# Kernel optimization log

Hardware: AMD Instinct MI355X
Metric: run time of the kernel (lower is better)

The kernel has to match this reference:

```python
import jax, jax.numpy as jnp
import numpy as np


def _conv1d(x, w, b, groups=1):
    # x: (B, Cin, N); w: (Cout, Cin//groups, K)
    pad = (w.shape[-1] - 1) // 2
    y = jax.lax.conv_general_dilated(
        x, w, window_strides=(1,), padding=[(pad, pad)],
        feature_group_count=groups, dimension_numbers=("NCH", "OIH", "NCH"))
    return y + b[None, :, None]


def _conv2d_1x1(x, w, b, groups=1):
    # x: (B, Cin, H, W); w: (Cout, Cin//groups, 1, 1)
    y = jax.lax.conv_general_dilated(
        x, w, window_strides=(1, 1), padding=[(0, 0), (0, 0)],
        feature_group_count=groups, dimension_numbers=("NCHW", "OIHW", "NCHW"))
    return y + b[None, :, None, None]


def setup_inputs() -> dict:
    key = jax.random.key(0)
    ks = jax.random.split(key, 13)
    B, C, N = 16, 256, 2048
    W, G = 128, 32  # width = 4 * groups
    s = 0.05
    inp = {"x": jax.random.normal(ks[0], (B, C, N), jnp.float32)}
    # tconvs: Conv1d(C,W,1) -> Conv1d(W,W,3,groups=G) -> Conv1d(W,C,1)
    inp["Wt1"] = jax.random.normal(ks[1], (W, C, 1), jnp.float32) * s
    inp["bt1"] = jax.random.normal(ks[2], (W,), jnp.float32) * s
    inp["Wt2"] = jax.random.normal(ks[3], (W, W // G, 3), jnp.float32) * s
    inp["bt2"] = jax.random.normal(ks[4], (W,), jnp.float32) * s
    inp["Wt3"] = jax.random.normal(ks[5], (C, W, 1), jnp.float32) * s
    inp["bt3"] = jax.random.normal(ks[6], (C,), jnp.float32) * s
    # sconvs: Conv2d(2C,W,1) -> Conv2d(W,W,1,groups=G) -> Conv2d(W,C,1)
    inp["Ws1"] = jax.random.normal(ks[7], (W, 2 * C, 1, 1), jnp.float32) * s
    inp["bs1"] = jax.random.normal(ks[8], (W,), jnp.float32) * s
    inp["Ws2"] = jax.random.normal(ks[9], (W, W // G, 1, 1), jnp.float32) * s
    inp["bs2"] = jax.random.normal(ks[10], (W,), jnp.float32) * s
    inp["Ws3"] = jax.random.normal(ks[11], (C, W, 1, 1), jnp.float32) * s
    inp["bs3"] = jax.random.normal(ks[12], (C,), jnp.float32) * s
    return inp


def reference(x, Wt1, bt1, Wt2, bt2, Wt3, bt3, Ws1, bs1, Ws2, bs2, Ws3, bs3):
    K, G = 3, 32
    B, C, N = x.shape
    # --- temporal branch (tconvs) ---
    t = jax.nn.relu(_conv1d(x, Wt1, bt1))
    t = jax.nn.relu(_conv1d(t, Wt2, bt2, groups=G))
    tout = _conv1d(t, Wt3, bt3)  # (B, C, N)
    # --- knn: pd[b,m,n] = -||x_m - x_n||^2; top-k largest = k nearest ---
    sq = jnp.sum(x * x, axis=1)  # (B, N)
    pd = 2.0 * jnp.einsum("bcm,bcn->bmn", x, x) - sq[:, :, None] - sq[:, None, :]
    idx = jax.lax.top_k(pd, K)[1]  # (B, N, K)
    # --- gather neighbors, style=1: cat(neighbor, center) ---
    xt = jnp.transpose(x, (0, 2, 1))  # (B, N, C)
    neigh = jax.vmap(lambda xb, ib: xb[ib])(xt, idx)  # (B, N, K, C)
    center = jnp.broadcast_to(xt[:, :, None, :], neigh.shape)
    feat = jnp.transpose(jnp.concatenate([neigh, center], axis=3), (0, 3, 1, 2))  # (B, 2C, N, K)
    # --- semantic branch (sconvs) + max over neighbors ---
    s1 = jax.nn.relu(_conv2d_1x1(feat, Ws1, bs1))
    s1 = jax.nn.relu(_conv2d_1x1(s1, Ws2, bs2, groups=G))
    sout = _conv2d_1x1(s1, Ws3, bs3).max(axis=-1)  # (B, C, N)
    return jax.nn.relu(tout + x + sout)
```

## Files before the change

### kernel.cpp

```cpp
#include <hip/hip_runtime.h>

#define DI __device__ __forceinline__

typedef float f4 __attribute__((ext_vector_type(4)));
typedef float f2 __attribute__((ext_vector_type(2)));
typedef unsigned short u16x8 __attribute__((ext_vector_type(8)));
typedef unsigned short u16x4 __attribute__((ext_vector_type(4)));
typedef __bf16 bf16x8 __attribute__((ext_vector_type(8)));
typedef float f32x4 __attribute__((ext_vector_type(4)));

constexpr int C = 256;
constexpr int N = 2048;
constexpr int BN = 16 * 2048;

DI float bf2f(unsigned short h){
  union { unsigned int u; float f; } v; v.u = ((unsigned int)h) << 16; return v.f;
}
DI unsigned short f2bf(float f){
  union { float f; unsigned int u; } v; v.f = f;
  unsigned int r = v.u + 0x7fffu + ((v.u >> 16) & 1u);
  return (unsigned short)(r >> 16);
}
DI unsigned int f2u(float f){ union { float f; unsigned int u; } v; v.f = f; return v.u; }
DI float u2f(unsigned int u){ union { unsigned int u; float f; } v; v.u = u; return v.f; }

DI void ins3(float v, int n, float& v0, float& v1, float& v2, int& i0, int& i1, int& i2){
  bool b0 = (v > v0) || (v == v0 && n < i0);
  bool b1 = (v > v1) || (v == v1 && n < i1);
  bool b2 = (v > v2) || (v == v2 && n < i2);
  if (b0){ v2=v1; i2=i1; v1=v0; i1=i0; v0=v; i0=n; }
  else if (b1){ v2=v1; i2=i1; v1=v; i1=n; }
  else if (b2){ v2=v; i2=n; }
}

DI void gload16(const void* g, void* l){
  __builtin_amdgcn_global_load_lds(
      (const __attribute__((address_space(1))) unsigned int*)g,
      (__attribute__((address_space(3))) unsigned int*)l, 16, 0, 0);
}

__global__ __launch_bounds__(256) void k_cvt(const float* __restrict__ x,
    unsigned short* __restrict__ xhT, float* __restrict__ xT, float* __restrict__ sq4)
{
  __shared__ float T[64][68];
  int bid = blockIdx.x;
  int pt = bid & 31, ct = (bid >> 5) & 3, b = bid >> 7;
  int p0 = pt * 64, c0 = ct * 64;
  int tid = threadIdx.x;
  int cr = tid >> 4, cv = tid & 15;
  const float* xb = x + ((size_t)b * C + c0) * N + p0;
  #pragma unroll
  for (int i = 0; i < 4; i++){
    int c = cr + i * 16;
    f4 v = *(const f4*)(xb + (size_t)c * N + cv * 4);
    T[cv*4+0][c] = v[0]; T[cv*4+1][c] = v[1]; T[cv*4+2][c] = v[2]; T[cv*4+3][c] = v[3];
  }
  __syncthreads();
  int p = tid >> 2, cq = tid & 3;
  size_t rowg = (size_t)b * N + p0 + p;
  float* xtr = xT + rowg * 256 + c0 + cq * 16;
  unsigned short* xhr = xhT + rowg * 256 + c0 + cq * 16;
  float sacc = 0.f;
  #pragma unroll
  for (int j = 0; j < 4; j++){
    f4 v = *(const f4*)&T[p][cq*16 + j*4];
    *(f4*)(xtr + j*4) = v;
    sacc += (v[0]*v[0] + v[1]*v[1]) + (v[2]*v[2] + v[3]*v[3]);
    u16x4 h; h[0]=f2bf(v[0]); h[1]=f2bf(v[1]); h[2]=f2bf(v[2]); h[3]=f2bf(v[3]);
    *(u16x4*)(xhr + j*4) = h;
  }
  sacc += __shfl_xor(sacc, 1, 64);
  sacc += __shfl_xor(sacc, 2, 64);
  if (cq == 0) sq4[rowg * 4 + ct] = sacc;
}

__global__ __launch_bounds__(256, 2) void k_pd(const unsigned short* __restrict__ xhT,
    const float* __restrict__ sq4, int* __restrict__ idx8)
{
  __shared__ __align__(16) char sm[81920];
  int wg = blockIdx.x;
  int wid = (wg & 7) * 64 + (wg >> 3);
  int b = wid >> 5, mt = wid & 31;
  int m0 = mt * 64;
  int tid = threadIdx.x, w = tid >> 6, l = tid & 63;
  const unsigned short* xb = xhT + (size_t)b * N * 256;
  const float* sqb4 = sq4 + (size_t)b * N * 4;
  char* Ab = sm + 49152;
  char* wbuf = sm + w * 12288;

  #pragma unroll
  for (int i = 0; i < 8; i++){
    int flat = i * 256 + tid;
    int m = flat >> 5, c = flat & 31;
    gload16(xb + (size_t)(m0 + m) * 256 + ((c ^ (m & 7)) << 3), Ab + flat * 16);
  }
  #pragma unroll
  for (int t = 0; t < 2; t++){
    #pragma unroll
    for (int i = 0; i < 4; i++){
      int p = i * 4 + (l >> 4), c = l & 15;
      gload16(xb + (size_t)(w * 16 + p) * 256 + t * 128 + ((c ^ (p & 7)) << 3),
              wbuf + t * 4096 + (i * 64 + l) * 16);
    }
  }
  asm volatile("s_waitcnt vmcnt(8)" ::: "memory");
  __builtin_amdgcn_s_barrier();

  bf16x8 af[4][8];
  #pragma unroll
  for (int rt = 0; rt < 4; rt++)
    #pragma unroll
    for (int ks = 0; ks < 8; ks++){
      int m = rt * 16 + (l & 15);
      int ch = ks * 4 + (l >> 4);
      af[rt][ks] = *(const bf16x8*)(Ab + m * 512 + ((ch ^ (m & 7)) << 4));
    }

  float K[16][3];
  #pragma unroll
  for (int a = 0; a < 16; a++){ K[a][0] = 0.f; K[a][1] = 0.f; K[a][2] = 0.f; }

  f32x4 acc[4];
  for (int it = 0; it < 64; it++){
    if (it < 62){
      int nx = it + 2;
      int P0 = (nx >> 1) * 64, kh2 = nx & 1;
      char* dst = wbuf + (nx % 3) * 4096;
      #pragma unroll
      for (int i = 0; i < 4; i++){
        int p = i * 4 + (l >> 4), c = l & 15;
        gload16(xb + (size_t)(P0 + w * 16 + p) * 256 + kh2 * 128 + ((c ^ (p & 7)) << 3),
                dst + (i * 64 + l) * 16);
      }
    }
    if (it < 62)       asm volatile("s_waitcnt vmcnt(8)" ::: "memory");
    else if (it == 62) asm volatile("s_waitcnt vmcnt(4)" ::: "memory");
    else               asm volatile("s_waitcnt vmcnt(0)" ::: "memory");

    const char* bb = wbuf + (it % 3) * 4096;
    int kh = it & 1;
    if (kh == 0){
      f32x4 z = {0.f, 0.f, 0.f, 0.f};
      #pragma unroll
      for (int rt = 0; rt < 4; rt++) acc[rt] = z;
    }
    #pragma unroll
    for (int ks = 0; ks < 4; ks++){
      int p = l & 15;
      int ch = ks * 4 + (l >> 4);
      bf16x8 bv = *(const bf16x8*)(bb + p * 256 + ((ch ^ (p & 7)) << 4));
      if (kh == 0){
        #pragma unroll
        for (int rt = 0; rt < 4; rt++)
          acc[rt] = __builtin_amdgcn_mfma_f32_16x16x32_bf16(af[rt][ks], bv, acc[rt], 0, 0, 0);
      } else {
        #pragma unroll
        for (int rt = 0; rt < 4; rt++)
          acc[rt] = __builtin_amdgcn_mfma_f32_16x16x32_bf16(af[rt][4 + ks], bv, acc[rt], 0, 0, 0);
      }
    }
    if (kh == 1){
      int col = (it >> 1) * 64 + w * 16 + (l & 15);
      f4 s4 = *(const f4*)(sqb4 + (size_t)col * 4);
      float nb = 1024.f - ((s4[0] + s4[1]) + (s4[2] + s4[3]));
      unsigned int ib = (unsigned int)(2047 - col);
      #pragma unroll
      for (int rt = 0; rt < 4; rt++)
        #pragma unroll
        for (int r = 0; r < 4; r++){
          float v = fmaf(acc[rt][r], 2.f, nb);
          float key = u2f((f2u(v) & 0xFFFFF800u) | ib);
          int a = rt * 4 + r;
          K[a][2] = __builtin_amdgcn_fmed3f(K[a][1], K[a][2], key);
          K[a][1] = __builtin_amdgcn_fmed3f(K[a][0], K[a][1], key);
          K[a][0] = fmaxf(K[a][0], key);
        }
    }
  }
  __syncthreads();
  float* mK = (float*)sm;
  #pragma unroll
  for (int rt = 0; rt < 4; rt++)
    #pragma unroll
    for (int r = 0; r < 4; r++){
      int row = rt * 16 + (l >> 4) * 4 + r;
      int base = row * 193 + w * 48 + (l & 15) * 3;
      mK[base+0] = K[rt*4+r][0]; mK[base+1] = K[rt*4+r][1]; mK[base+2] = K[rt*4+r][2];
    }
  __syncthreads();
  float* aux = (float*)(sm + 49408);
  {
    int row = tid >> 2, q = tid & 3;
    float t0 = 0.f, t1 = 0.f, t2 = 0.f, t3 = 0.f;
    const float* src = mK + row * 193 + q * 48;
    for (int s = 0; s < 48; s++){
      float v = src[s];
      t3 = __builtin_amdgcn_fmed3f(t2, t3, v);
      t2 = __builtin_amdgcn_fmed3f(t1, t2, v);
      t1 = __builtin_amdgcn_fmed3f(t0, t1, v);
      t0 = fmaxf(t0, v);
    }
    float* d = aux + row * 17 + q * 4;
    d[0] = t0; d[1] = t1; d[2] = t2; d[3] = t3;
  }
  __syncthreads();
  if (tid < 64){
    float u0=0.f,u1=0.f,u2=0.f,u3=0.f,u4=0.f,u5=0.f,u6=0.f,u7=0.f;
    const float* srcp = aux + tid * 17;
    #pragma unroll
    for (int s = 0; s < 16; s++){
      float v = srcp[s];
      u7 = __builtin_amdgcn_fmed3f(u6, u7, v);
      u6 = __builtin_amdgcn_fmed3f(u5, u6, v);
      u5 = __builtin_amdgcn_fmed3f(u4, u5, v);
      u4 = __builtin_amdgcn_fmed3f(u3, u4, v);
      u3 = __builtin_amdgcn_fmed3f(u2, u3, v);
      u2 = __builtin_amdgcn_fmed3f(u1, u2, v);
      u1 = __builtin_amdgcn_fmed3f(u0, u1, v);
      u0 = fmaxf(u0, v);
    }
    int* d = idx8 + ((size_t)(b * N + m0 + tid)) * 8;
    d[0]=2047-(int)(f2u(u0)&2047u); d[1]=2047-(int)(f2u(u1)&2047u);
    d[2]=2047-(int)(f2u(u2)&2047u); d[3]=2047-(int)(f2u(u3)&2047u);
    d[4]=2047-(int)(f2u(u4)&2047u); d[5]=2047-(int)(f2u(u5)&2047u);
    d[6]=2047-(int)(f2u(u6)&2047u); d[7]=2047-(int)(f2u(u7)&2047u);
  }
}

__global__ __launch_bounds__(256) void k_rerank(const float* __restrict__ xT,
    const float* __restrict__ sq4, const int* __restrict__ idx8, int* __restrict__ idx3)
{
  int w = threadIdx.x >> 6, l = threadIdx.x & 63;
  int h = l >> 5, lh = l & 31;
  int wv = blockIdx.x * 4 + w;
  #pragma unroll
  for (int rr = 0; rr < 2; rr++){
    int row = wv * 2 + rr;
    int b = row >> 11;
    const float* xm = xT + (size_t)row * 256 + lh * 8;
    f4 xm0 = *(const f4*)xm;
    f4 xm1 = *(const f4*)(xm + 4);
    const int* cb = idx8 + (size_t)row * 8;
    int nn[8];
    #pragma unroll
    for (int c2 = 0; c2 < 8; c2++) nn[c2] = cb[c2];
    f4 a0[4], a1[4];
    #pragma unroll
    for (int j = 0; j < 4; j++){
      int n = nn[2*j + h];
      const float* xn = xT + ((size_t)(b * N + n)) * 256 + lh * 8;
      a0[j] = *(const f4*)xn;
      a1[j] = *(const f4*)(xn + 4);
    }
    float v0=-3e38f, v1=v0, v2=v0; int i0=0x7fffffff, i1=i0, i2=i0;
    #pragma unroll
    for (int j = 0; j < 4; j++){
      float s = ((xm0[0]*a0[j][0] + xm0[1]*a0[j][1]) + (xm0[2]*a0[j][2] + xm0[3]*a0[j][3]))
              + ((xm1[0]*a1[j][0] + xm1[1]*a1[j][1]) + (xm1[2]*a1[j][2] + xm1[3]*a1[j][3]));
      #pragma unroll
      for (int d = 1; d < 32; d <<= 1) s += __shfl_xor(s, d, 64);
      float so = __shfl_xor(s, 32, 64);
      float pe = h ? so : s;
      float po = h ? s : so;
      int ne = nn[2*j], no = nn[2*j+1];
      f4 s4e = *(const f4*)(sq4 + ((size_t)(b * N + ne)) * 4);
      f4 s4o = *(const f4*)(sq4 + ((size_t)(b * N + no)) * 4);
      float ve = 2.f * pe - ((s4e[0] + s4e[1]) + (s4e[2] + s4e[3]));
      float vo = 2.f * po - ((s4o[0] + s4o[1]) + (s4o[2] + s4o[3]));
      ins3(ve, ne, v0, v1, v2, i0, i1, i2);
      ins3(vo, no, v0, v1, v2, i0, i1, i2);
    }
    if (l == 0){
      size_t ob = (size_t)row * 3;
      idx3[ob] = i0; idx3[ob+1] = i1; idx3[ob+2] = i2;
    }
  }
}

__global__ __launch_bounds__(256, 2) void k_ut1(const float* __restrict__ Ws1,
    const float* __restrict__ Wt1, const float* __restrict__ bt1,
    const unsigned short* __restrict__ xhT,
    unsigned short* __restrict__ u_ws, unsigned short* __restrict__ t1_ws)
{
  __shared__ __align__(16) unsigned short A[64 * 256];
  int wg = blockIdx.x;
  int wid = (wg & 7) * 96 + (wg >> 3);
  int mb = wid % 6, pt = wid / 6;
  int m0 = mb * 64, p0 = pt * 256;
  int tid = threadIdx.x, w = tid >> 6, l = tid & 63;
  #pragma unroll
  for (int i = 0; i < 8; i++){
    int flat = i * 256 + tid;
    int m = flat >> 5, c = flat & 31;
    int mg = m0 + m;
    const float* srcp;
    if (mg < 128)      srcp = Ws1 + (size_t)mg * 512 + c * 8;
    else if (mg < 256) srcp = Ws1 + (size_t)(mg - 128) * 512 + 256 + c * 8;
    else               srcp = Wt1 + (size_t)(mg - 256) * 256 + c * 8;
    f4 v0 = *(const f4*)srcp, v1 = *(const f4*)(srcp + 4);
    u16x8 h;
    h[0]=f2bf(v0[0]); h[1]=f2bf(v0[1]); h[2]=f2bf(v0[2]); h[3]=f2bf(v0[3]);
    h[4]=f2bf(v1[0]); h[5]=f2bf(v1[1]); h[6]=f2bf(v1[2]); h[7]=f2bf(v1[3]);
    *(u16x8*)(A + m * 256 + ((c ^ (m & 7)) << 3)) = h;
  }
  __syncthreads();
  bf16x8 af[4][8];
  #pragma unroll
  for (int rt = 0; rt < 4; rt++)
    #pragma unroll
    for (int ks = 0; ks < 8; ks++){
      int m = rt * 16 + (l & 15);
      int ch = ks * 4 + (l >> 4);
      af[rt][ks] = *(const bf16x8*)((const char*)A + m * 512 + ((ch ^ (m & 7)) << 4));
    }
  bool isU = (m0 < 256);
  f4 bias[4];
  if (!isU){
    #pragma unroll
    for (int rt = 0; rt < 4; rt++)
      bias[rt] = *(const f4*)(bt1 + (m0 - 256) + rt * 16 + (l >> 4) * 4);
  }
  for (int ct = 0; ct < 4; ct++){
    int p = p0 + ct * 64 + w * 16 + (l & 15);
    const unsigned short* bp = xhT + (size_t)p * 256 + (l >> 4) * 8;
    f32x4 acc[4];
    f32x4 z = {0.f, 0.f, 0.f, 0.f};
    #pragma unroll
    for (int rt = 0; rt < 4; rt++) acc[rt] = z;
    #pragma unroll
    for (int ks = 0; ks < 8; ks++){
      bf16x8 bv = *(const bf16x8*)(bp + ks * 32);
      #pragma unroll
      for (int rt = 0; rt < 4; rt++)
        acc[rt] = __builtin_amdgcn_mfma_f32_16x16x32_bf16(af[rt][ks], bv, acc[rt], 0, 0, 0);
    }
    if (isU){
      #pragma unroll
      for (int rt = 0; rt < 4; rt++){
        u16x4 h;
        h[0]=f2bf(acc[rt][0]); h[1]=f2bf(acc[rt][1]); h[2]=f2bf(acc[rt][2]); h[3]=f2bf(acc[rt][3]);
        *(u16x4*)(u_ws + (size_t)p * 256 + m0 + rt * 16 + (l >> 4) * 4) = h;
      }
    } else {
      #pragma unroll
      for (int rt = 0; rt < 4; rt++){
        u16x4 h;
        h[0]=f2bf(fmaxf(acc[rt][0] + bias[rt][0], 0.f));
        h[1]=f2bf(fmaxf(acc[rt][1] + bias[rt][1], 0.f));
        h[2]=f2bf(fmaxf(acc[rt][2] + bias[rt][2], 0.f));
        h[3]=f2bf(fmaxf(acc[rt][3] + bias[rt][3], 0.f));
        *(u16x4*)(t1_ws + (size_t)p * 128 + (m0 - 256) + rt * 16 + (l >> 4) * 4) = h;
      }
    }
  }
}

__global__ __launch_bounds__(256) void k_te(const unsigned short* __restrict__ t1_ws,
    const float* __restrict__ Wt2, const float* __restrict__ bt2,
    unsigned short* __restrict__ t2_ws,
    const unsigned short* __restrict__ u_ws, const int* __restrict__ idx_ws,
    const float* __restrict__ bs1, const float* __restrict__ Ws2,
    const float* __restrict__ bs2, unsigned short* __restrict__ s2_ws)
{
  __shared__ float w2[1536];
  __shared__ float b2[128];
  __shared__ float sb1[128], sb2[128], sw2[512];
  int tid = threadIdx.x;
  if (blockIdx.x < 512){
    for (int i = tid; i < 1536; i += 256) w2[i] = Wt2[i];
    if (tid < 128) b2[tid] = bt2[tid];
    __syncthreads();
    int p = blockIdx.x * 64 + (tid >> 2);
    int q = tid & 3;
    int n = p & (N - 1);
    const unsigned short* rp = t1_ws + (size_t)p * 128;
    u16x8 zz = {0,0,0,0,0,0,0,0};
    #pragma unroll
    for (int g8 = 0; g8 < 4; g8++){
      int ch0 = q*32 + g8*8;
      u16x8 vm1 = (n > 0)     ? *(const u16x8*)(rp - 128 + ch0) : zz;
      u16x8 v0  =               *(const u16x8*)(rp + ch0);
      u16x8 vp1 = (n < N - 1) ? *(const u16x8*)(rp + 128 + ch0) : zz;
      float fm1[8], f0[8], fp1[8];
      #pragma unroll
      for (int e = 0; e < 8; e++){ fm1[e]=bf2f(vm1[e]); f0[e]=bf2f(v0[e]); fp1[e]=bf2f(vp1[e]); }
      u16x8 o;
      #pragma unroll
      for (int j = 0; j < 8; j++){
        int wch = ch0 + j, gb = j & ~3;
        float acc = b2[wch];
        #pragma unroll
        for (int i = 0; i < 4; i++){
          acc += w2[wch*12 + i*3 + 0] * fm1[gb + i];
          acc += w2[wch*12 + i*3 + 1] * f0[gb + i];
          acc += w2[wch*12 + i*3 + 2] * fp1[gb + i];
        }
        o[j] = f2bf(fmaxf(acc, 0.f));
      }
      *(u16x8*)(t2_ws + (size_t)p * 128 + ch0) = o;
    }
  } else {
    if (tid < 128){ sb1[tid] = bs1[tid]; sb2[tid] = bs2[tid]; }
    sw2[tid] = Ws2[tid]; sw2[tid+256] = Ws2[tid+256];
    __syncthreads();
    int p0 = (blockIdx.x - 512) * 64;
    #pragma unroll
    for (int rep = 0; rep < 3; rep++){
      int task = rep*256 + tid;
      int r = task >> 2, q = task & 3;
      int pl = r / 3, k = r - pl*3;
      int p = p0 + pl;
      int b = p >> 11;
      int m = idx_ws[(size_t)p*3 + k] & (N - 1);
      const unsigned short* ua = u_ws + ((size_t)(b*N + m))*256 + q*32;
      const unsigned short* ub = u_ws + ((size_t)p)*256 + 128 + q*32;
      float s1v[32];
      #pragma unroll
      for (int jj = 0; jj < 4; jj++){
        u16x8 a  = *(const u16x8*)(ua + jj*8);
        u16x8 cbv = *(const u16x8*)(ub + jj*8);
        #pragma unroll
        for (int e = 0; e < 8; e++){
          int j = jj*8 + e;
          s1v[j] = fmaxf(bf2f(a[e]) + bf2f(cbv[e]) + sb1[q*32 + j], 0.f);
        }
      }
      #pragma unroll
      for (int jj = 0; jj < 4; jj++){
        u16x8 o;
        #pragma unroll
        for (int e = 0; e < 8; e++){
          int j = jj*8 + e;
          int ch = q*32 + j, gb = j & ~3;
          float a2 = sb2[ch] + sw2[ch*4+0]*s1v[gb]   + sw2[ch*4+1]*s1v[gb+1]
                             + sw2[ch*4+2]*s1v[gb+2] + sw2[ch*4+3]*s1v[gb+3];
          o[e] = f2bf(fmaxf(a2, 0.f));
        }
        *(u16x8*)(s2_ws + ((size_t)k * BN + p) * 128 + q*32 + jj*8) = o;
      }
    }
  }
}

__global__ __launch_bounds__(256, 2) void k_e2f(const unsigned short* __restrict__ s2_ws,
    const unsigned short* __restrict__ t2_ws,
    const float* __restrict__ Ws3, const float* __restrict__ bs3,
    const float* __restrict__ Wt3, const float* __restrict__ bt3,
    const float* __restrict__ x, float* __restrict__ out)
{
  __shared__ __align__(16) unsigned short As[64 * 128];
  __shared__ __align__(16) unsigned short At[64 * 128];
  int wg = blockIdx.x;
  int wid = (wg & 7) * 64 + (wg >> 3);
  int mb = wid & 3, pt = wid >> 2;
  int m0 = mb * 64, p0 = pt * 256;
  int tid = threadIdx.x, w = tid >> 6, l = tid & 63;
  #pragma unroll
  for (int i = 0; i < 4; i++){
    int flat = i * 256 + tid;
    int m = flat >> 4, c = flat & 15;
    {
      const float* srcp = Ws3 + (size_t)(m0 + m) * 128 + c * 8;
      f4 v0 = *(const f4*)srcp, v1 = *(const f4*)(srcp + 4);
      u16x8 h;
      h[0]=f2bf(v0[0]); h[1]=f2bf(v0[1]); h[2]=f2bf(v0[2]); h[3]=f2bf(v0[3]);
      h[4]=f2bf(v1[0]); h[5]=f2bf(v1[1]); h[6]=f2bf(v1[2]); h[7]=f2bf(v1[3]);
      *(u16x8*)(As + m * 128 + ((c ^ (m & 7)) << 3)) = h;
    }
    {
      const float* srcp = Wt3 + (size_t)(m0 + m) * 128 + c * 8;
      f4 v0 = *(const f4*)srcp, v1 = *(const f4*)(srcp + 4);
      u16x8 h;
      h[0]=f2bf(v0[0]); h[1]=f2bf(v0[1]); h[2]=f2bf(v0[2]); h[3]=f2bf(v0[3]);
      h[4]=f2bf(v1[0]); h[5]=f2bf(v1[1]); h[6]=f2bf(v1[2]); h[7]=f2bf(v1[3]);
      *(u16x8*)(At + m * 128 + ((c ^ (m & 7)) << 3)) = h;
    }
  }
  __syncthreads();
  bf16x8 afs[4][4], aft[4][4];
  #pragma unroll
  for (int rt = 0; rt < 4; rt++)
    #pragma unroll
    for (int ks = 0; ks < 4; ks++){
      int m = rt * 16 + (l & 15);
      int ch = ks * 4 + (l >> 4);
      afs[rt][ks] = *(const bf16x8*)((const char*)As + m * 256 + ((ch ^ (m & 7)) << 4));
      aft[rt][ks] = *(const bf16x8*)((const char*)At + m * 256 + ((ch ^ (m & 7)) << 4));
    }
  f4 biasS[4], biasT[4];
  #pragma unroll
  for (int rt = 0; rt < 4; rt++){
    biasS[rt] = *(const f4*)(bs3 + m0 + rt * 16 + (l >> 4) * 4);
    biasT[rt] = *(const f4*)(bt3 + m0 + rt * 16 + (l >> 4) * 4);
  }
  for (int ct = 0; ct < 4; ct++){
    int p = p0 + ct * 64 + w * 16 + (l & 15);
    int b = p >> 11, n = p & (N - 1);
    const unsigned short* bp0 = s2_ws + ((size_t)(0 * BN + p)) * 128 + (l >> 4) * 8;
    const unsigned short* bp1 = s2_ws + ((size_t)(1 * BN + p)) * 128 + (l >> 4) * 8;
    const unsigned short* bp2 = s2_ws + ((size_t)(2 * BN + p)) * 128 + (l >> 4) * 8;
    const unsigned short* bpt = t2_ws + ((size_t)p) * 128 + (l >> 4) * 8;
    f32x4 acc[4][4];
    f32x4 z = {0.f, 0.f, 0.f, 0.f};
    #pragma unroll
    for (int rt = 0; rt < 4; rt++){ acc[rt][0]=z; acc[rt][1]=z; acc[rt][2]=z; acc[rt][3]=z; }
    #pragma unroll
    for (int ks = 0; ks < 4; ks++){
      bf16x8 bv0 = *(const bf16x8*)(bp0 + ks * 32);
      bf16x8 bv1 = *(const bf16x8*)(bp1 + ks * 32);
      bf16x8 bv2 = *(const bf16x8*)(bp2 + ks * 32);
      bf16x8 bvt = *(const bf16x8*)(bpt + ks * 32);
      #pragma unroll
      for (int rt = 0; rt < 4; rt++){
        acc[rt][0] = __builtin_amdgcn_mfma_f32_16x16x32_bf16(afs[rt][ks], bv0, acc[rt][0], 0, 0, 0);
        acc[rt][1] = __builtin_amdgcn_mfma_f32_16x16x32_bf16(afs[rt][ks], bv1, acc[rt][1], 0, 0, 0);
        acc[rt][2] = __builtin_amdgcn_mfma_f32_16x16x32_bf16(afs[rt][ks], bv2, acc[rt][2], 0, 0, 0);
        acc[rt][3] = __builtin_amdgcn_mfma_f32_16x16x32_bf16(aft[rt][ks], bvt, acc[rt][3], 0, 0, 0);
      }
    }
    #pragma unroll
    for (int rt = 0; rt < 4; rt++){
      int mbase = m0 + rt * 16 + (l >> 4) * 4;
      #pragma unroll
      for (int r = 0; r < 4; r++){
        float sout = fmaxf(fmaxf(acc[rt][0][r], acc[rt][1][r]), acc[rt][2][r]) + biasS[rt][r];
        float tout = acc[rt][3][r] + biasT[rt][r];
        size_t ob = ((size_t)(b * 256 + mbase + r)) * N + n;
        out[ob] = fmaxf(sout + tout + x[ob], 0.f);
      }
    }
  }
}

extern "C" void kernel_launch(void* const* d_in, const int* in_sizes, int n_in,
                              void* d_out, int out_size, void* d_ws, size_t ws_size,
                              hipStream_t stream)
{
  const float* x   = (const float*)d_in[0];
  const float* Wt1 = (const float*)d_in[1];
  const float* bt1 = (const float*)d_in[2];
  const float* Wt2 = (const float*)d_in[3];
  const float* bt2 = (const float*)d_in[4];
  const float* Wt3 = (const float*)d_in[5];
  const float* bt3 = (const float*)d_in[6];
  const float* Ws1 = (const float*)d_in[7];
  const float* bs1 = (const float*)d_in[8];
  const float* Ws2 = (const float*)d_in[9];
  const float* bs2 = (const float*)d_in[10];
  const float* Ws3 = (const float*)d_in[11];
  const float* bs3 = (const float*)d_in[12];
  float* out = (float*)d_out;

  char* ws = (char*)d_ws;
  if (ws_size < 59244544u) return;
  int*   idx3 = (int*)ws;
  char*  P    = ws + 524288;
  float*          xT    = (float*)P;
  unsigned short* xhT   = (unsigned short*)(P + 33554432);
  int*            idx8  = (int*)(P + 50331648);
  float*          sq4   = (float*)(P + 51380224);
  unsigned short* u_ws  = (unsigned short*)P;
  unsigned short* t1_ws = (unsigned short*)(P + 16777216);
  unsigned short* t2_ws = (unsigned short*)(P + 25165824);
  unsigned short* s2_ws = (unsigned short*)(P + 33554432);

  k_cvt   <<<2048, 256, 0, stream>>>(x, xhT, xT, sq4);
  k_pd    <<<512, 256, 0, stream>>>(xhT, sq4, idx8);
  k_rerank<<<4096, 256, 0, stream>>>(xT, sq4, idx8, idx3);
  k_ut1   <<<768, 256, 0, stream>>>(Ws1, Wt1, bt1, xhT, u_ws, t1_ws);
  k_te    <<<1024, 256, 0, stream>>>(t1_ws, Wt2, bt2, t2_ws, u_ws, idx3, bs1, Ws2, bs2, s2_ws);
  k_e2f   <<<512, 256, 0, stream>>>(s2_ws, t2_ws, Ws3, bs3, Wt3, bt3, x, out);
}
```

Measured before the change: 252.1 us.

## Halve k_pd row tile to 32 rows and double-buffer for higher occupancy

The pairwise-distance/top-k kernel now handles 32 query rows per workgroup instead of 64, doubling the grid to 1024 blocks. It shrinks LDS from 80KB to 48KB, switches the per-wave B prefetch from a triple buffer to a double buffer, and halves register fragments and top-k state, so the launch bound can allow 3 blocks per CU. The aim is more latency hiding and better fill across CUs. The cost is that every column tile is reloaded twice as often, doubling global and L2 traffic for the B operand, and the prefetch distance is shorter.

```diff
diff --git a/kernel.cpp b/kernel.cpp
--- a/kernel.cpp
+++ b/kernel.cpp
@@ -74,75 +74,72 @@
   if (cq == 0) sq4[rowg * 4 + ct] = sacc;
 }
 
-__global__ __launch_bounds__(256, 2) void k_pd(const unsigned short* __restrict__ xhT,
+__global__ __launch_bounds__(256, 3) void k_pd(const unsigned short* __restrict__ xhT,
     const float* __restrict__ sq4, int* __restrict__ idx8)
 {
-  __shared__ __align__(16) char sm[81920];
+  __shared__ __align__(16) char sm[49152];
   int wg = blockIdx.x;
-  int wid = (wg & 7) * 64 + (wg >> 3);
-  int b = wid >> 5, mt = wid & 31;
-  int m0 = mt * 64;
+  int wid = (wg & 7) * 128 + (wg >> 3);
+  int b = wid >> 6, mt = wid & 63;
+  int m0 = mt * 32;
   int tid = threadIdx.x, w = tid >> 6, l = tid & 63;
   const unsigned short* xb = xhT + (size_t)b * N * 256;
   const float* sqb4 = sq4 + (size_t)b * N * 4;
-  char* Ab = sm + 49152;
-  char* wbuf = sm + w * 12288;
-
-  #pragma unroll
-  for (int i = 0; i < 8; i++){
+  char* Ab = sm + 32768;
+  char* wbuf = sm + w * 8192;
+
+  #pragma unroll
+  for (int i = 0; i < 4; i++){
     int flat = i * 256 + tid;
     int m = flat >> 5, c = flat & 31;
     gload16(xb + (size_t)(m0 + m) * 256 + ((c ^ (m & 7)) << 3), Ab + flat * 16);
   }
   #pragma unroll
-  for (int t = 0; t < 2; t++){
-    #pragma unroll
-    for (int i = 0; i < 4; i++){
-      int p = i * 4 + (l >> 4), c = l & 15;
-      gload16(xb + (size_t)(w * 16 + p) * 256 + t * 128 + ((c ^ (p & 7)) << 3),
-              wbuf + t * 4096 + (i * 64 + l) * 16);
-    }
-  }
-  asm volatile("s_waitcnt vmcnt(8)" ::: "memory");
+  for (int i = 0; i < 4; i++){
+    int p = i * 4 + (l >> 4), c = l & 15;
+    gload16(xb + (size_t)(w * 16 + p) * 256 + ((c ^ (p & 7)) << 3),
+            wbuf + (i * 64 + l) * 16);
+  }
+  asm volatile("s_waitcnt vmcnt(4)" ::: "memory");
   __builtin_amdgcn_s_barrier();
 
-  bf16x8 af[4][8];
-  #pragma unroll
-  for (int rt = 0; rt < 4; rt++)
+  bf16x8 af[2][8];
+  #pragma unroll
+  for (int rt = 0; rt < 2; rt++)
     #pragma unroll
     for (int ks = 0; ks < 8; ks++){
       int m = rt * 16 + (l & 15);
       int ch = ks * 4 + (l >> 4);
       af[rt][ks] = *(const bf16x8*)(Ab + m * 512 + ((ch ^ (m & 7)) << 4));
-    }
-
-  float K[16][3];
-  #pragma unroll
-  for (int a = 0; a < 16; a++){ K[a][0] = 0.f; K[a][1] = 0.f; K[a][2] = 0.f; }
-
-  f32x4 acc[4];
+      asm volatile("" : "+v"(af[rt][ks]));
+    }
+
+  float K[8][3];
+  #pragma unroll
+  for (int a = 0; a < 8; a++){ K[a][0] = 0.f; K[a][1] = 0.f; K[a][2] = 0.f; }
+
+  f32x4 acc[2];
   for (int it = 0; it < 64; it++){
-    if (it < 62){
-      int nx = it + 2;
+    if (it + 1 < 64){
+      int nx = it + 1;
       int P0 = (nx >> 1) * 64, kh2 = nx & 1;
-      char* dst = wbuf + (nx % 3) * 4096;
+      char* dst = wbuf + (nx & 1) * 4096;
       #pragma unroll
       for (int i = 0; i < 4; i++){
         int p = i * 4 + (l >> 4), c = l & 15;
         gload16(xb + (size_t)(P0 + w * 16 + p) * 256 + kh2 * 128 + ((c ^ (p & 7)) << 3),
                 dst + (i * 64 + l) * 16);
       }
-    }
-    if (it < 62)       asm volatile("s_waitcnt vmcnt(8)" ::: "memory");
-    else if (it == 62) asm volatile("s_waitcnt vmcnt(4)" ::: "memory");
-    else               asm volatile("s_waitcnt vmcnt(0)" ::: "memory");
-
-    const char* bb = wbuf + (it % 3) * 4096;
+      asm volatile("s_waitcnt vmcnt(4)" ::: "memory");
+    } else {
+      asm volatile("s_waitcnt vmcnt(0)" ::: "memory");
+    }
+
+    const char* bb = wbuf + (it & 1) * 4096;
     int kh = it & 1;
     if (kh == 0){
       f32x4 z = {0.f, 0.f, 0.f, 0.f};
-      #pragma unroll
-      for (int rt = 0; rt < 4; rt++) acc[rt] = z;
+      acc[0] = z; acc[1] = z;
     }
     #pragma unroll
     for (int ks = 0; ks < 4; ks++){
@@ -150,13 +147,11 @@
       int ch = ks * 4 + (l >> 4);
       bf16x8 bv = *(const bf16x8*)(bb + p * 256 + ((ch ^ (p & 7)) << 4));
       if (kh == 0){
-        #pragma unroll
-        for (int rt = 0; rt < 4; rt++)
-          acc[rt] = __builtin_amdgcn_mfma_f32_16x16x32_bf16(af[rt][ks], bv, acc[rt], 0, 0, 0);
+        acc[0] = __builtin_amdgcn_mfma_f32_16x16x32_bf16(af[0][ks], bv, acc[0], 0, 0, 0);
+        acc[1] = __builtin_amdgcn_mfma_f32_16x16x32_bf16(af[1][ks], bv, acc[1], 0, 0, 0);
       } else {
-        #pragma unroll
-        for (int rt = 0; rt < 4; rt++)
-          acc[rt] = __builtin_amdgcn_mfma_f32_16x16x32_bf16(af[rt][4 + ks], bv, acc[rt], 0, 0, 0);
+        acc[0] = __builtin_amdgcn_mfma_f32_16x16x32_bf16(af[0][4 + ks], bv, acc[0], 0, 0, 0);
+        acc[1] = __builtin_amdgcn_mfma_f32_16x16x32_bf16(af[1][4 + ks], bv, acc[1], 0, 0, 0);
       }
     }
     if (kh == 1){
@@ -165,7 +160,7 @@
       float nb = 1024.f - ((s4[0] + s4[1]) + (s4[2] + s4[3]));
       unsigned int ib = (unsigned int)(2047 - col);
       #pragma unroll
-      for (int rt = 0; rt < 4; rt++)
+      for (int rt = 0; rt < 2; rt++)
         #pragma unroll
         for (int r = 0; r < 4; r++){
           float v = fmaf(acc[rt][r], 2.f, nb);
@@ -180,7 +175,7 @@
   __syncthreads();
   float* mK = (float*)sm;
   #pragma unroll
-  for (int rt = 0; rt < 4; rt++)
+  for (int rt = 0; rt < 2; rt++)
     #pragma unroll
     for (int r = 0; r < 4; r++){
       int row = rt * 16 + (l >> 4) * 4 + r;
@@ -188,8 +183,8 @@
       mK[base+0] = K[rt*4+r][0]; mK[base+1] = K[rt*4+r][1]; mK[base+2] = K[rt*4+r][2];
     }
   __syncthreads();
-  float* aux = (float*)(sm + 49408);
-  {
+  float* aux = (float*)(sm + 24704);
+  if (tid < 128){
     int row = tid >> 2, q = tid & 3;
     float t0 = 0.f, t1 = 0.f, t2 = 0.f, t3 = 0.f;
     const float* src = mK + row * 193 + q * 48;
@@ -204,7 +199,7 @@
     d[0] = t0; d[1] = t1; d[2] = t2; d[3] = t3;
   }
   __syncthreads();
-  if (tid < 64){
+  if (tid < 32){
     float u0=0.f,u1=0.f,u2=0.f,u3=0.f,u4=0.f,u5=0.f,u6=0.f,u7=0.f;
     const float* srcp = aux + tid * 17;
     #pragma unroll
@@ -565,7 +560,7 @@
   unsigned short* s2_ws = (unsigned short*)(P + 33554432);
 
   k_cvt   <<<2048, 256, 0, stream>>>(x, xhT, xT, sq4);
-  k_pd    <<<512, 256, 0, stream>>>(xhT, sq4, idx8);
+  k_pd    <<<1024, 256, 0, stream>>>(xhT, sq4, idx8);
   k_rerank<<<4096, 256, 0, stream>>>(xT, sq4, idx8, idx3);
   k_ut1   <<<768, 256, 0, stream>>>(Ws1, Wt1, bt1, xhT, u_ws, t1_ws);
   k_te    <<<1024, 256, 0, stream>>>(t1_ws, Wt2, bt2, t2_ws, u_ws, idx3, bs1, Ws2, bs2, s2_ws);
```

New measurement: 266.0 us. +5.5%, slower.
